# Kernel optimization log

Measured on AMD Instinct MI355X. Metric: run time of the kernel, lower is better.

Reference implementation:

```python
import jax, jax.numpy as jnp
import numpy as np

B, T, HID, NH = 2, 2048, 1024, 16
HD = HID // NH  # head_dim = 64
ROPE_BASE = 1000000.0


def _precompute_freqs(dim, end, rope_base):
    inv = 1.0 / (rope_base ** (np.arange(0, dim, 2)[: dim // 2].astype(np.float32) / dim))
    t = np.arange(end, dtype=np.float32)
    freqs = np.outer(t, inv).astype(np.float32)  # (end, dim//2)
    cos = np.concatenate([np.cos(freqs), np.cos(freqs)], axis=-1)
    sin = np.concatenate([np.sin(freqs), np.sin(freqs)], axis=-1)
    return jnp.asarray(cos), jnp.asarray(sin)


def setup_inputs() -> dict:
    key = jax.random.key(0)
    ks = jax.random.split(key, 5)
    x = jax.random.normal(ks[0], (B, T, HID), dtype=jnp.float32)
    s = 1.0 / np.sqrt(HID)
    Wq = jax.random.normal(ks[1], (HID, HID), dtype=jnp.float32) * s
    Wk = jax.random.normal(ks[2], (HID, HID), dtype=jnp.float32) * s
    Wv = jax.random.normal(ks[3], (HID, HID), dtype=jnp.float32) * s
    Wo = jax.random.normal(ks[4], (HID, HID), dtype=jnp.float32) * s
    cos, sin = _precompute_freqs(HD, T, ROPE_BASE)
    return {"x": x, "Wq": Wq, "Wk": Wk, "Wv": Wv, "Wo": Wo, "cos": cos, "sin": sin}


def _rotate_half(u):
    half = u.shape[-1] // 2
    return jnp.concatenate([-u[..., half:], u[..., :half]], axis=-1)


def reference(x, Wq, Wk, Wv, Wo, cos, sin):
    b, t, _ = x.shape
    # projections (nn.Linear: x @ W.T)
    q = (x @ Wq.T).reshape(b, t, NH, HD).transpose(0, 2, 1, 3)  # (B,H,T,D)
    k = (x @ Wk.T).reshape(b, t, NH, HD).transpose(0, 2, 1, 3)
    v = (x @ Wv.T).reshape(b, t, NH, HD).transpose(0, 2, 1, 3)
    c = cos[None, None, :t, :]
    s = sin[None, None, :t, :]
    q = q * c + _rotate_half(q) * s
    k = k * c + _rotate_half(k) * s
    scores = jnp.einsum("bhqd,bhkd->bhqk", q, k) / jnp.sqrt(jnp.float32(HD))
    causal = jnp.tril(jnp.ones((t, t), dtype=bool))
    scores = jnp.where(causal[None, None], scores, jnp.float32(-jnp.inf))
    prob = jax.nn.softmax(scores, axis=-1)
    out = jnp.einsum("bhqk,bhkd->bhqd", prob, v)
    out = out.transpose(0, 2, 1, 3).reshape(b, t, HID)
    return out @ Wo.T
```

## Files before the change

kernel.cpp:

```cpp
#include <hip/hip_runtime.h>
#include <hip/hip_bf16.h>

#define B_   2
#define T_   2048
#define HID_ 1024
#define NH_  16
#define HD_  64
#define K_   1024
#define M_   (B_*T_)

typedef __attribute__((ext_vector_type(8)))  short bf16x8;
typedef __attribute__((ext_vector_type(4)))  float f32x4;
typedef __attribute__((ext_vector_type(16))) float f32x16;
typedef __attribute__((ext_vector_type(4)))  unsigned int u32x4;
typedef __attribute__((ext_vector_type(2)))  unsigned int u32x2;

#define LOG2E 1.44269504088896340736f

__device__ inline unsigned short f2bf(float f) {
    __hip_bfloat16 h = __float2bfloat16(f);
    return __builtin_bit_cast(unsigned short, h);
}
__device__ inline unsigned int pk2(float a, float b) {
    return (unsigned int)f2bf(a) | ((unsigned int)f2bf(b) << 16);
}
__device__ inline unsigned int pkt(float a, float b) {
    return __builtin_amdgcn_perm(__builtin_bit_cast(unsigned, a),
                                 __builtin_bit_cast(unsigned, b), 0x03020706u);
}
__device__ inline bf16x8 cvt8(float4 a, float4 b) {
    bf16x8 r;
    r[0]=(short)f2bf(a.x); r[1]=(short)f2bf(a.y); r[2]=(short)f2bf(a.z); r[3]=(short)f2bf(a.w);
    r[4]=(short)f2bf(b.x); r[5]=(short)f2bf(b.y); r[6]=(short)f2bf(b.z); r[7]=(short)f2bf(b.w);
    return r;
}

__global__ __launch_bounds__(256)
void cast_all(const float* __restrict__ x,
              const float* __restrict__ W0, const float* __restrict__ W1,
              const float* __restrict__ W2, const float* __restrict__ W3,
              unsigned short* __restrict__ xo,
              unsigned short* __restrict__ o0, unsigned short* __restrict__ o1,
              unsigned short* __restrict__ o2, unsigned short* __restrict__ o3) {
    const int blk = blockIdx.x;
    const float* in;
    unsigned short* out;
    int i;
    if (blk < 2048) {
        in = x; out = xo; i = blk * 256 + threadIdx.x;
    } else {
        const int wb = blk - 2048, sec = wb >> 9;
        in  = (sec == 0) ? W0 : (sec == 1) ? W1 : (sec == 2) ? W2 : W3;
        out = (sec == 0) ? o0 : (sec == 1) ? o1 : (sec == 2) ? o2 : o3;
        i = (wb & 511) * 256 + threadIdx.x;
    }
    float4 a = ((const float4*)in)[2*i], b = ((const float4*)in)[2*i + 1];
    ((bf16x8*)out)[i] = cvt8(a, b);
}

template<int TYPE>
__global__ __launch_bounds__(256)
void gemm_k(const unsigned short* __restrict__ A, const unsigned short* __restrict__ W0,
            const unsigned short* __restrict__ W1, const unsigned short* __restrict__ W2,
            const float* __restrict__ cs, const float* __restrict__ sn,
            unsigned short* __restrict__ qb, unsigned short* __restrict__ kb,
            unsigned short* __restrict__ vtb, float* __restrict__ fout) {
    __shared__ unsigned short As[128*64];
    __shared__ unsigned short Bs[128*64];
    const int tid = threadIdx.x;
    const int w = tid >> 6, lane = tid & 63;
    const int u = lane >> 4, c = lane & 15;
    const int bm = blockIdx.x * 128, bn = blockIdx.y * 128;
    const int wm = (w & 1) * 64, wn = (w >> 1) * 64;
    const int srow = tid >> 3, scol = (tid & 7) << 3;

    const unsigned short* Wsec;
    int wrowbase;
    if constexpr (TYPE == 0) {
        const int sec = bn >> 10;
        Wsec = (sec == 0) ? W0 : ((sec == 1) ? W1 : W2);
        wrowbase = bn & 1023;
    } else {
        Wsec = W0;
        wrowbase = bn;
    }
    const unsigned short* Wp = Wsec + (size_t)(wrowbase + srow) * K_ + scol;
    const unsigned short* Ap = A + (size_t)(bm + srow) * K_ + scol;

    f32x4 acc[4][4] = {};
    bf16x8 ra[4], rb[4];

    auto loadin = [&](int k0) {
        #pragma unroll
        for (int i = 0; i < 4; ++i) {
            ra[i] = *(const bf16x8*)(Ap + (size_t)i * 32 * K_ + k0);
            rb[i] = *(const bf16x8*)(Wp + (size_t)i * 32 * K_ + k0);
        }
    };
    loadin(0);

    for (int k0 = 0; k0 < K_; k0 += 64) {
        __syncthreads();
        #pragma unroll
        for (int i = 0; i < 4; ++i) {
            const int row = i * 32 + srow;
            const int sc = (scol * 2) ^ ((row & 7) << 4);
            *(bf16x8*)((char*)As + row * 128 + sc) = ra[i];
            *(bf16x8*)((char*)Bs + row * 128 + sc) = rb[i];
        }
        __syncthreads();
        if (k0 < K_ - 64) loadin(k0 + 64);
        #pragma unroll
        for (int kk = 0; kk < 2; ++kk) {
            bf16x8 af[4], bfr[4];
            #pragma unroll
            for (int mi = 0; mi < 4; ++mi) {
                const int row = wm + mi * 16 + c;
                const int sc = (kk * 64 + u * 16) ^ ((row & 7) << 4);
                af[mi] = *(const bf16x8*)((char*)As + row * 128 + sc);
            }
            #pragma unroll
            for (int ni = 0; ni < 4; ++ni) {
                const int row = wn + ni * 16 + c;
                const int sc = (kk * 64 + u * 16) ^ ((row & 7) << 4);
                bfr[ni] = *(const bf16x8*)((char*)Bs + row * 128 + sc);
            }
            #pragma unroll
            for (int mi = 0; mi < 4; ++mi)
                #pragma unroll
                for (int ni = 0; ni < 4; ++ni)
                    acc[mi][ni] = __builtin_amdgcn_mfma_f32_16x16x32_bf16(
                        af[mi], bfr[ni], acc[mi][ni], 0, 0, 0);
        }
    }

    if constexpr (TYPE == 1) {
        #pragma unroll
        for (int mi = 0; mi < 4; ++mi)
            #pragma unroll
            for (int ni = 0; ni < 4; ++ni)
                #pragma unroll
                for (int r = 0; r < 4; ++r)
                    fout[(size_t)(bm + wm + 16*mi + 4*u + r) * HID_ + (bn + wn + 16*ni + c)] =
                        acc[mi][ni][r];
    } else {
        const int sec = bn >> 10;
        const int h = ((bn + wn) & 1023) >> 6;
        if (sec == 2) {
            #pragma unroll
            for (int mi = 0; mi < 4; ++mi)
                #pragma unroll
                for (int r = 0; r < 4; ++r) {
                    const int mg = bm + wm + 16*mi + 4*u + r;
                    const int bb = mg >> 11, t = mg & 2047;
                    const int tk = (t & ~12) | ((t & 4) << 1) | ((t & 8) >> 1);
                    #pragma unroll
                    for (int ni = 0; ni < 4; ++ni)
                        vtb[((size_t)(bb*16 + h) * 64 + 16*ni + c) * 2048 + tk] =
                            f2bf(acc[mi][ni][r]);
                }
        } else {
            unsigned short* ob = sec ? kb : qb;
            const float qsc = sec ? 1.0f : (0.125f * LOG2E);
            #pragma unroll
            for (int mi = 0; mi < 4; ++mi)
                #pragma unroll
                for (int r = 0; r < 4; ++r) {
                    const int mg = bm + wm + 16*mi + 4*u + r;
                    const int bb = mg >> 11, t = mg & 2047;
                    const size_t base = ((size_t)(bb*16 + h) * 2048 + t) * 64;
                    #pragma unroll
                    for (int ni = 0; ni < 2; ++ni) {
                        const int dlo = 16*ni + c;
                        const float cv = cs[t*64 + dlo], sv = sn[t*64 + dlo];
                        const float Aa = acc[mi][ni][r], Bb = acc[mi][ni+2][r];
                        ob[base + dlo]      = f2bf((Aa*cv - Bb*sv) * qsc);
                        ob[base + dlo + 32] = f2bf((Bb*cv + Aa*sv) * qsc);
                    }
                }
        }
    }
}

__global__ __launch_bounds__(256)
void attn11(const unsigned short* __restrict__ q, const unsigned short* __restrict__ k,
            const unsigned short* __restrict__ vt, unsigned short* __restrict__ ab) {
    const int raw = blockIdx.x;
    const int bh   = (raw & 7) + 8 * ((raw >> 3) & 3);
    const int qblk = 63 - (raw >> 5);
    const int tid = threadIdx.x;
    const int wid = tid >> 6, lane = tid & 63;
    const int h = lane >> 5, c = lane & 31;
    const int b = bh >> 4, hh = bh & 15;
    const int q0 = qblk * 32;
    const int qgc = q0 + c;
    const unsigned short* qp = q  + (size_t)bh * (T_*64);
    const unsigned short* kp = k  + (size_t)bh * (T_*64);
    const unsigned short* vp = vt + (size_t)bh * (64*T_);

    const int kloff  = c * 64 + 8 * h;
    const int vloff0 = c * 2048 + 8 * h;
    const int vloff1 = vloff0 + 32 * 2048;

    bf16x8 qf[4];
    {
        const unsigned short* qrow = qp + (q0 + c) * 64 + 8 * h;
        #pragma unroll
        for (int s = 0; s < 4; ++s)
            qf[s] = *(const bf16x8*)(qrow + s * 16);
    }

    f32x16 O0 = {}, O1 = {};
    float m = -1e30f, lsum = 0.f;
    const int nst = qblk + 1;

    auto loadKV = [&](bf16x8 (&kf)[4], bf16x8 (&vf)[4], int st) {
        const unsigned short* kst = kp + (st << 11);
        const unsigned short* vst = vp + (st << 5);
        #pragma unroll
        for (int s = 0; s < 4; ++s)
            kf[s] = *(const bf16x8*)(kst + kloff + s * 16);
        vf[0] = *(const bf16x8*)(vst + vloff0);
        vf[1] = *(const bf16x8*)(vst + vloff0 + 16);
        vf[2] = *(const bf16x8*)(vst + vloff1);
        vf[3] = *(const bf16x8*)(vst + vloff1 + 16);
    };

    auto process = [&](const bf16x8 (&kf)[4], const bf16x8 (&vf)[4], int st) {
        const int kvs = st << 5;
        __builtin_amdgcn_s_setprio(1);
        f32x16 sa = {};
        #pragma unroll
        for (int s = 0; s < 4; ++s)
            sa = __builtin_amdgcn_mfma_f32_32x32x16_bf16(kf[s], qf[s], sa, 0, 0, 0);
        __builtin_amdgcn_s_setprio(0);
        float p[16];
        #pragma unroll
        for (int r = 0; r < 16; ++r) p[r] = sa[r];
        if (st == qblk) {
            #pragma unroll
            for (int r = 0; r < 16; ++r) {
                const int kk = kvs + (r & 3) + 8 * (r >> 2) + 4 * h;
                if (kk > qgc) p[r] = -1e30f;
            }
        }
        const float a0 = fmaxf(fmaxf(p[0],  p[1]),  p[2]);
        const float a1 = fmaxf(fmaxf(p[3],  p[4]),  p[5]);
        const float a2 = fmaxf(fmaxf(p[6],  p[7]),  p[8]);
        const float a3 = fmaxf(fmaxf(p[9],  p[10]), p[11]);
        const float a4 = fmaxf(fmaxf(p[12], p[13]), p[14]);
        float mx = fmaxf(fmaxf(fmaxf(a0, a1), fmaxf(a2, a3)), fmaxf(a4, p[15]));
        if (!__all(mx <= m + 8.0f)) {
            mx = fmaxf(mx, __shfl_xor(mx, 32));
            const float mn = fmaxf(m, mx);
            const float f = __builtin_amdgcn_exp2f(m - mn);
            m = mn;
            lsum *= f;
            #pragma unroll
            for (int r = 0; r < 16; ++r) { O0[r] *= f; O1[r] *= f; }
        }
        float ps = 0.f;
        #pragma unroll
        for (int r = 0; r < 16; ++r) {
            p[r] = __builtin_amdgcn_exp2f(p[r] - m);
            ps += p[r];
        }
        lsum += ps;
        u32x4 B0w = { pkt(p[0],  p[1]),  pkt(p[2],  p[3]),
                      pkt(p[4],  p[5]),  pkt(p[6],  p[7])  };
        u32x4 B1w = { pkt(p[8],  p[9]),  pkt(p[10], p[11]),
                      pkt(p[12], p[13]), pkt(p[14], p[15]) };
        bf16x8 PB0 = __builtin_bit_cast(bf16x8, B0w);
        bf16x8 PB1 = __builtin_bit_cast(bf16x8, B1w);
        __builtin_amdgcn_s_setprio(1);
        O0 = __builtin_amdgcn_mfma_f32_32x32x16_bf16(vf[0], PB0, O0, 0, 0, 0);
        O0 = __builtin_amdgcn_mfma_f32_32x32x16_bf16(vf[1], PB1, O0, 0, 0, 0);
        O1 = __builtin_amdgcn_mfma_f32_32x32x16_bf16(vf[2], PB0, O1, 0, 0, 0);
        O1 = __builtin_amdgcn_mfma_f32_32x32x16_bf16(vf[3], PB1, O1, 0, 0, 0);
        __builtin_amdgcn_s_setprio(0);
    };

    bf16x8 kA[4], kB[4], vA[4], vB[4];
    if (wid < nst) loadKV(kA, vA, wid);
    for (int st = wid; st < nst; st += 8) {
        if (st + 4 < nst) loadKV(kB, vB, st + 4);
        process(kA, vA, st);
        if (st + 4 >= nst) break;
        if (st + 8 < nst) loadKV(kA, vA, st + 8);
        process(kB, vB, st + 4);
    }
    lsum += __shfl_xor(lsum, 32);

    __shared__ unsigned OSu[4][32 * 34];
    __shared__ float mS[4][32], lS[4][32];
    if (h == 0) { mS[wid][c] = m; lS[wid][c] = lsum; }
    {
        unsigned* os = &OSu[wid][0];
        const int rb = c * 34 + 2 * h;
        #pragma unroll
        for (int j = 0; j < 4; ++j) {
            os[rb + 4*j]          = pk2(O0[4*j],   O0[4*j+1]);
            os[rb + 4*j + 1]      = pk2(O0[4*j+2], O0[4*j+3]);
            os[rb + 16 + 4*j]     = pk2(O1[4*j],   O1[4*j+1]);
            os[rb + 16 + 4*j + 1] = pk2(O1[4*j+2], O1[4*j+3]);
        }
    }
    __syncthreads();

    const int ql = tid & 31, ug = (tid >> 5) * 4;
    const float M = fmaxf(fmaxf(mS[0][ql], mS[1][ql]), fmaxf(mS[2][ql], mS[3][ql]));
    float acc[8] = {};
    float L = 0.f;
    #pragma unroll
    for (int w2 = 0; w2 < 4; ++w2) {
        const float sc = __builtin_amdgcn_exp2f(mS[w2][ql] - M);
        L += lS[w2][ql] * sc;
        u32x2 pa = *(u32x2*)&OSu[w2][ql * 34 + ug];
        u32x2 pb = *(u32x2*)&OSu[w2][ql * 34 + ug + 2];
        #pragma unroll
        for (int t = 0; t < 2; ++t) {
            acc[2*t]     += __builtin_bit_cast(float, pa[t] << 16) * sc;
            acc[2*t+1]   += __builtin_bit_cast(float, pa[t] & 0xffff0000u) * sc;
            acc[4+2*t]   += __builtin_bit_cast(float, pb[t] << 16) * sc;
            acc[4+2*t+1] += __builtin_bit_cast(float, pb[t] & 0xffff0000u) * sc;
        }
    }
    const float inv = 1.0f / L;
    uint4 ov;
    ov.x = pk2(acc[0]*inv, acc[1]*inv);
    ov.y = pk2(acc[2]*inv, acc[3]*inv);
    ov.z = pk2(acc[4]*inv, acc[5]*inv);
    ov.w = pk2(acc[6]*inv, acc[7]*inv);
    *(uint4*)(ab + ((size_t)(b * T_) + q0 + ql) * HID_ + hh * 64 + ug * 2) = ov;
}

extern "C" void kernel_launch(void* const* d_in, const int* in_sizes, int n_in,
                              void* d_out, int out_size, void* d_ws, size_t ws_size,
                              hipStream_t stream) {
    const float* x  = (const float*)d_in[0];
    const float* Wq = (const float*)d_in[1];
    const float* Wk = (const float*)d_in[2];
    const float* Wv = (const float*)d_in[3];
    const float* Wo = (const float*)d_in[4];
    const float* cs = (const float*)d_in[5];
    const float* sn = (const float*)d_in[6];
    char* wsb = (char*)d_ws;
    unsigned short* xb  = (unsigned short*)(wsb);
    unsigned short* wqb = (unsigned short*)(wsb + (8u  << 20));
    unsigned short* wkb = (unsigned short*)(wsb + (10u << 20));
    unsigned short* wvb = (unsigned short*)(wsb + (12u << 20));
    unsigned short* wob = (unsigned short*)(wsb + (14u << 20));
    unsigned short* qb  = (unsigned short*)(wsb + (16u << 20));
    unsigned short* kb  = (unsigned short*)(wsb + (24u << 20));
    unsigned short* vtb = (unsigned short*)(wsb + (32u << 20));
    unsigned short* ab  = (unsigned short*)(wsb + (40u << 20));

    cast_all<<<4096, 256, 0, stream>>>(x, Wq, Wk, Wv, Wo, xb, wqb, wkb, wvb, wob);

    gemm_k<0><<<dim3(M_/128, 3072/128), 256, 0, stream>>>(
        xb, wqb, wkb, wvb, cs, sn, qb, kb, vtb, nullptr);
    attn11<<<2048, 256, 0, stream>>>(qb, kb, vtb, ab);
    gemm_k<1><<<dim3(M_/128, HID_/128), 256, 0, stream>>>(
        ab, wob, nullptr, nullptr, nullptr, nullptr,
        nullptr, nullptr, nullptr, (float*)d_out);
}
```

Measured before the change: 127.8 us.

## Process three query tiles per attention block, remap GEMM blocks across XCDs

The attention kernel now has each block handle 96 query rows as three 32-row tiles that share one K/V load per key step. This cuts K/V global traffic and block count (704 blocks instead of 2048), at the cost of more registers and uneven causal work per tile. Both GEMMs move to a 1D grid with an XCD-aware swizzle of block indices, meant to improve L2 locality. The output projection GEMM also switches to 128x64 tiles so it launches more blocks.

```diff
diff --git a/kernel.cpp b/kernel.cpp
--- a/kernel.cpp
+++ b/kernel.cpp
@@ -65,13 +65,26 @@
             const float* __restrict__ cs, const float* __restrict__ sn,
             unsigned short* __restrict__ qb, unsigned short* __restrict__ kb,
             unsigned short* __restrict__ vtb, float* __restrict__ fout) {
+    constexpr int BN = (TYPE == 1) ? 64 : 128;
+    constexpr int NB = BN / 32;
+    constexpr int NF = BN / 32;
     __shared__ unsigned short As[128*64];
-    __shared__ unsigned short Bs[128*64];
+    __shared__ unsigned short Bs[BN*64];
     const int tid = threadIdx.x;
     const int w = tid >> 6, lane = tid & 63;
     const int u = lane >> 4, c = lane & 15;
-    const int bm = blockIdx.x * 128, bn = blockIdx.y * 128;
-    const int wm = (w & 1) * 64, wn = (w >> 1) * 64;
+    const int bid = blockIdx.x;
+    const int xcd = bid & 7, idx = bid >> 3;
+    int bmi, bni;
+    if constexpr (TYPE == 0) {
+        bmi = (xcd & 3) * 8 + (idx & 7);
+        bni = (xcd >> 2) * 12 + (idx >> 3);
+    } else {
+        bmi = (xcd & 3) * 8 + (idx & 7);
+        bni = (xcd >> 2) * 8 + (idx >> 3);
+    }
+    const int bm = bmi * 128, bn = bni * BN;
+    const int wm = (w & 1) * 64, wn = (w >> 1) * (BN / 2);
     const int srow = tid >> 3, scol = (tid & 7) << 3;
 
     const unsigned short* Wsec;
@@ -87,15 +100,16 @@
     const unsigned short* Wp = Wsec + (size_t)(wrowbase + srow) * K_ + scol;
     const unsigned short* Ap = A + (size_t)(bm + srow) * K_ + scol;
 
-    f32x4 acc[4][4] = {};
-    bf16x8 ra[4], rb[4];
+    f32x4 acc[4][NF] = {};
+    bf16x8 ra[4], rb[NB];
 
     auto loadin = [&](int k0) {
         #pragma unroll
-        for (int i = 0; i < 4; ++i) {
+        for (int i = 0; i < 4; ++i)
             ra[i] = *(const bf16x8*)(Ap + (size_t)i * 32 * K_ + k0);
+        #pragma unroll
+        for (int i = 0; i < NB; ++i)
             rb[i] = *(const bf16x8*)(Wp + (size_t)i * 32 * K_ + k0);
-        }
     };
     loadin(0);
 
@@ -106,13 +120,18 @@
             const int row = i * 32 + srow;
             const int sc = (scol * 2) ^ ((row & 7) << 4);
             *(bf16x8*)((char*)As + row * 128 + sc) = ra[i];
+        }
+        #pragma unroll
+        for (int i = 0; i < NB; ++i) {
+            const int row = i * 32 + srow;
+            const int sc = (scol * 2) ^ ((row & 7) << 4);
             *(bf16x8*)((char*)Bs + row * 128 + sc) = rb[i];
         }
         __syncthreads();
         if (k0 < K_ - 64) loadin(k0 + 64);
         #pragma unroll
         for (int kk = 0; kk < 2; ++kk) {
-            bf16x8 af[4], bfr[4];
+            bf16x8 af[4], bfr[NF];
             #pragma unroll
             for (int mi = 0; mi < 4; ++mi) {
                 const int row = wm + mi * 16 + c;
@@ -120,7 +139,7 @@
                 af[mi] = *(const bf16x8*)((char*)As + row * 128 + sc);
             }
             #pragma unroll
-            for (int ni = 0; ni < 4; ++ni) {
+            for (int ni = 0; ni < NF; ++ni) {
                 const int row = wn + ni * 16 + c;
                 const int sc = (kk * 64 + u * 16) ^ ((row & 7) << 4);
                 bfr[ni] = *(const bf16x8*)((char*)Bs + row * 128 + sc);
@@ -128,7 +147,7 @@
             #pragma unroll
             for (int mi = 0; mi < 4; ++mi)
                 #pragma unroll
-                for (int ni = 0; ni < 4; ++ni)
+                for (int ni = 0; ni < NF; ++ni)
                     acc[mi][ni] = __builtin_amdgcn_mfma_f32_16x16x32_bf16(
                         af[mi], bfr[ni], acc[mi][ni], 0, 0, 0);
         }
@@ -138,7 +157,7 @@
         #pragma unroll
         for (int mi = 0; mi < 4; ++mi)
             #pragma unroll
-            for (int ni = 0; ni < 4; ++ni)
+            for (int ni = 0; ni < NF; ++ni)
                 #pragma unroll
                 for (int r = 0; r < 4; ++r)
                     fout[(size_t)(bm + wm + 16*mi + 4*u + r) * HID_ + (bn + wn + 16*ni + c)] =
@@ -183,17 +202,21 @@
 }
 
 __global__ __launch_bounds__(256)
-void attn11(const unsigned short* __restrict__ q, const unsigned short* __restrict__ k,
+void attn17(const unsigned short* __restrict__ q, const unsigned short* __restrict__ k,
             const unsigned short* __restrict__ vt, unsigned short* __restrict__ ab) {
     const int raw = blockIdx.x;
-    const int bh   = (raw & 7) + 8 * ((raw >> 3) & 3);
-    const int qblk = 63 - (raw >> 5);
+    const int bh     = (raw & 7) + 8 * ((raw >> 3) & 3);
+    const int qchunk = 21 - (raw >> 5);
+    const bool hasBC = (qchunk < 21);
     const int tid = threadIdx.x;
     const int wid = tid >> 6, lane = tid & 63;
     const int h = lane >> 5, c = lane & 31;
     const int b = bh >> 4, hh = bh & 15;
-    const int q0 = qblk * 32;
-    const int qgc = q0 + c;
+    const int q0 = qchunk * 96;
+    const int qgcA = q0 + c, qgcB = q0 + 32 + c, qgcC = q0 + 64 + c;
+    const int stAd = 3 * qchunk;
+    const int stBd = stAd + 1, stCd = stAd + 2;
+    const int NT   = hasBC ? (stAd + 3) : (stAd + 1);
     const unsigned short* qp = q  + (size_t)bh * (T_*64);
     const unsigned short* kp = k  + (size_t)bh * (T_*64);
     const unsigned short* vp = vt + (size_t)bh * (64*T_);
@@ -202,42 +225,39 @@
     const int vloff0 = c * 2048 + 8 * h;
     const int vloff1 = vloff0 + 32 * 2048;
 
-    bf16x8 qf[4];
+    bf16x8 qfA[4], qfB[4], qfC[4];
     {
-        const unsigned short* qrow = qp + (q0 + c) * 64 + 8 * h;
-        #pragma unroll
-        for (int s = 0; s < 4; ++s)
-            qf[s] = *(const bf16x8*)(qrow + s * 16);
-    }
-
-    f32x16 O0 = {}, O1 = {};
-    float m = -1e30f, lsum = 0.f;
-    const int nst = qblk + 1;
-
-    auto loadKV = [&](bf16x8 (&kf)[4], bf16x8 (&vf)[4], int st) {
+        const unsigned short* qrowA = qp + (q0 + c) * 64 + 8 * h;
+        #pragma unroll
+        for (int s = 0; s < 4; ++s) qfA[s] = *(const bf16x8*)(qrowA + s * 16);
+        if (hasBC) {
+            #pragma unroll
+            for (int s = 0; s < 4; ++s) {
+                qfB[s] = *(const bf16x8*)(qrowA + 32 * 64 + s * 16);
+                qfC[s] = *(const bf16x8*)(qrowA + 64 * 64 + s * 16);
+            }
+        }
+    }
+
+    f32x16 OA0 = {}, OA1 = {}, OB0 = {}, OB1 = {}, OC0 = {}, OC1 = {};
+    float mA = -1e30f, lA = 0.f, mB = -1e30f, lB = 0.f, mC = -1e30f, lC = 0.f;
+
+    auto loadK = [&](bf16x8 (&kf)[4], int st) {
         const unsigned short* kst = kp + (st << 11);
-        const unsigned short* vst = vp + (st << 5);
         #pragma unroll
         for (int s = 0; s < 4; ++s)
             kf[s] = *(const bf16x8*)(kst + kloff + s * 16);
-        vf[0] = *(const bf16x8*)(vst + vloff0);
-        vf[1] = *(const bf16x8*)(vst + vloff0 + 16);
-        vf[2] = *(const bf16x8*)(vst + vloff1);
-        vf[3] = *(const bf16x8*)(vst + vloff1 + 16);
     };
 
-    auto process = [&](const bf16x8 (&kf)[4], const bf16x8 (&vf)[4], int st) {
+    auto tileRest = [&](f32x16 sa, int st, int std_, int qgc,
+                        float& m, float& l, f32x16& O0, f32x16& O1,
+                        const bf16x8& vf0, const bf16x8& vf1,
+                        const bf16x8& vf2, const bf16x8& vf3) {
         const int kvs = st << 5;
-        __builtin_amdgcn_s_setprio(1);
-        f32x16 sa = {};
-        #pragma unroll
-        for (int s = 0; s < 4; ++s)
-            sa = __builtin_amdgcn_mfma_f32_32x32x16_bf16(kf[s], qf[s], sa, 0, 0, 0);
-        __builtin_amdgcn_s_setprio(0);
         float p[16];
         #pragma unroll
         for (int r = 0; r < 16; ++r) p[r] = sa[r];
-        if (st == qblk) {
+        if (st == std_) {
             #pragma unroll
             for (int r = 0; r < 16; ++r) {
                 const int kk = kvs + (r & 3) + 8 * (r >> 2) + 4 * h;
@@ -254,8 +274,7 @@
             mx = fmaxf(mx, __shfl_xor(mx, 32));
             const float mn = fmaxf(m, mx);
             const float f = __builtin_amdgcn_exp2f(m - mn);
-            m = mn;
-            lsum *= f;
+            m = mn; l *= f;
             #pragma unroll
             for (int r = 0; r < 16; ++r) { O0[r] *= f; O1[r] *= f; }
         }
@@ -265,7 +284,7 @@
             p[r] = __builtin_amdgcn_exp2f(p[r] - m);
             ps += p[r];
         }
-        lsum += ps;
+        l += ps;
         u32x4 B0w = { pkt(p[0],  p[1]),  pkt(p[2],  p[3]),
                       pkt(p[4],  p[5]),  pkt(p[6],  p[7])  };
         u32x4 B1w = { pkt(p[8],  p[9]),  pkt(p[10], p[11]),
@@ -273,65 +292,111 @@
         bf16x8 PB0 = __builtin_bit_cast(bf16x8, B0w);
         bf16x8 PB1 = __builtin_bit_cast(bf16x8, B1w);
         __builtin_amdgcn_s_setprio(1);
-        O0 = __builtin_amdgcn_mfma_f32_32x32x16_bf16(vf[0], PB0, O0, 0, 0, 0);
-        O0 = __builtin_amdgcn_mfma_f32_32x32x16_bf16(vf[1], PB1, O0, 0, 0, 0);
-        O1 = __builtin_amdgcn_mfma_f32_32x32x16_bf16(vf[2], PB0, O1, 0, 0, 0);
-        O1 = __builtin_amdgcn_mfma_f32_32x32x16_bf16(vf[3], PB1, O1, 0, 0, 0);
+        O0 = __builtin_amdgcn_mfma_f32_32x32x16_bf16(vf0, PB0, O0, 0, 0, 0);
+        O0 = __builtin_amdgcn_mfma_f32_32x32x16_bf16(vf1, PB1, O0, 0, 0, 0);
+        O1 = __builtin_amdgcn_mfma_f32_32x32x16_bf16(vf2, PB0, O1, 0, 0, 0);
+        O1 = __builtin_amdgcn_mfma_f32_32x32x16_bf16(vf3, PB1, O1, 0, 0, 0);
         __builtin_amdgcn_s_setprio(0);
     };
 
-    bf16x8 kA[4], kB[4], vA[4], vB[4];
-    if (wid < nst) loadKV(kA, vA, wid);
-    for (int st = wid; st < nst; st += 8) {
-        if (st + 4 < nst) loadKV(kB, vB, st + 4);
-        process(kA, vA, st);
-        if (st + 4 >= nst) break;
-        if (st + 8 < nst) loadKV(kA, vA, st + 8);
-        process(kB, vB, st + 4);
-    }
-    lsum += __shfl_xor(lsum, 32);
-
-    __shared__ unsigned OSu[4][32 * 34];
-    __shared__ float mS[4][32], lS[4][32];
-    if (h == 0) { mS[wid][c] = m; lS[wid][c] = lsum; }
+    auto qkt = [&](const bf16x8 (&kf)[4], const bf16x8 (&qf)[4]) -> f32x16 {
+        __builtin_amdgcn_s_setprio(1);
+        f32x16 sa = {};
+        #pragma unroll
+        for (int s = 0; s < 4; ++s)
+            sa = __builtin_amdgcn_mfma_f32_32x32x16_bf16(kf[s], qf[s], sa, 0, 0, 0);
+        __builtin_amdgcn_s_setprio(0);
+        return sa;
+    };
+
+    bf16x8 kf_[4];
+    if (wid < NT) {
+        loadK(kf_, wid);
+        for (int st = wid; st < NT; st += 4) {
+            const unsigned short* vst = vp + (st << 5);
+            bf16x8 vf0 = *(const bf16x8*)(vst + vloff0);
+            bf16x8 vf1 = *(const bf16x8*)(vst + vloff0 + 16);
+            bf16x8 vf2 = *(const bf16x8*)(vst + vloff1);
+            bf16x8 vf3 = *(const bf16x8*)(vst + vloff1 + 16);
+            const bool doA = (st <= stAd);
+            const bool doB = hasBC && (st <= stBd);
+            if (doA) {
+                f32x16 sa = qkt(kf_, qfA);
+                if (!hasBC && st + 4 < NT) loadK(kf_, st + 4);
+                tileRest(sa, st, stAd, qgcA, mA, lA, OA0, OA1, vf0, vf1, vf2, vf3);
+            }
+            if (doB) {
+                f32x16 sa = qkt(kf_, qfB);
+                tileRest(sa, st, stBd, qgcB, mB, lB, OB0, OB1, vf0, vf1, vf2, vf3);
+            }
+            if (hasBC) {
+                f32x16 sa = qkt(kf_, qfC);
+                if (st + 4 < NT) loadK(kf_, st + 4);
+                tileRest(sa, st, stCd, qgcC, mC, lC, OC0, OC1, vf0, vf1, vf2, vf3);
+            }
+        }
+    }
+    lA += __shfl_xor(lA, 32);
+    lB += __shfl_xor(lB, 32);
+    lC += __shfl_xor(lC, 32);
+
+    __shared__ unsigned OSu[4][96 * 34];
+    __shared__ float mS[4][96], lS[4][96];
+    if (h == 0) {
+        mS[wid][c] = mA;      lS[wid][c] = lA;
+        mS[wid][32 + c] = mB; lS[wid][32 + c] = lB;
+        mS[wid][64 + c] = mC; lS[wid][64 + c] = lC;
+    }
     {
         unsigned* os = &OSu[wid][0];
-        const int rb = c * 34 + 2 * h;
+        const int rbA = c * 34 + 2 * h;
+        const int rbB = (32 + c) * 34 + 2 * h;
+        const int rbC = (64 + c) * 34 + 2 * h;
         #pragma unroll
         for (int j = 0; j < 4; ++j) {
-            os[rb + 4*j]          = pk2(O0[4*j],   O0[4*j+1]);
-            os[rb + 4*j + 1]      = pk2(O0[4*j+2], O0[4*j+3]);
-            os[rb + 16 + 4*j]     = pk2(O1[4*j],   O1[4*j+1]);
-            os[rb + 16 + 4*j + 1] = pk2(O1[4*j+2], O1[4*j+3]);
+            os[rbA + 4*j]          = pk2(OA0[4*j],   OA0[4*j+1]);
+            os[rbA + 4*j + 1]      = pk2(OA0[4*j+2], OA0[4*j+3]);
+            os[rbA + 16 + 4*j]     = pk2(OA1[4*j],   OA1[4*j+1]);
+            os[rbA + 16 + 4*j + 1] = pk2(OA1[4*j+2], OA1[4*j+3]);
+            os[rbB + 4*j]          = pk2(OB0[4*j],   OB0[4*j+1]);
+            os[rbB + 4*j + 1]      = pk2(OB0[4*j+2], OB0[4*j+3]);
+            os[rbB + 16 + 4*j]     = pk2(OB1[4*j],   OB1[4*j+1]);
+            os[rbB + 16 + 4*j + 1] = pk2(OB1[4*j+2], OB1[4*j+3]);
+            os[rbC + 4*j]          = pk2(OC0[4*j],   OC0[4*j+1]);
+            os[rbC + 4*j + 1]      = pk2(OC0[4*j+2], OC0[4*j+3]);
+            os[rbC + 16 + 4*j]     = pk2(OC1[4*j],   OC1[4*j+1]);
+            os[rbC + 16 + 4*j + 1] = pk2(OC1[4*j+2], OC1[4*j+3]);
         }
     }
     __syncthreads();
 
-    const int ql = tid & 31, ug = (tid >> 5) * 4;
-    const float M = fmaxf(fmaxf(mS[0][ql], mS[1][ql]), fmaxf(mS[2][ql], mS[3][ql]));
-    float acc[8] = {};
-    float L = 0.f;
     #pragma unroll
-    for (int w2 = 0; w2 < 4; ++w2) {
-        const float sc = __builtin_amdgcn_exp2f(mS[w2][ql] - M);
-        L += lS[w2][ql] * sc;
-        u32x2 pa = *(u32x2*)&OSu[w2][ql * 34 + ug];
-        u32x2 pb = *(u32x2*)&OSu[w2][ql * 34 + ug + 2];
-        #pragma unroll
-        for (int t = 0; t < 2; ++t) {
-            acc[2*t]     += __builtin_bit_cast(float, pa[t] << 16) * sc;
-            acc[2*t+1]   += __builtin_bit_cast(float, pa[t] & 0xffff0000u) * sc;
-            acc[4+2*t]   += __builtin_bit_cast(float, pb[t] << 16) * sc;
-            acc[4+2*t+1] += __builtin_bit_cast(float, pb[t] & 0xffff0000u) * sc;
-        }
-    }
-    const float inv = 1.0f / L;
-    uint4 ov;
-    ov.x = pk2(acc[0]*inv, acc[1]*inv);
-    ov.y = pk2(acc[2]*inv, acc[3]*inv);
-    ov.z = pk2(acc[4]*inv, acc[5]*inv);
-    ov.w = pk2(acc[6]*inv, acc[7]*inv);
-    *(uint4*)(ab + ((size_t)(b * T_) + q0 + ql) * HID_ + hh * 64 + ug * 2) = ov;
+    for (int rr = 0; rr < 3; ++rr) {
+        if (rr > 0 && !hasBC) break;
+        const int rl = rr * 32 + (tid & 31);
+        const int ug = (tid >> 5) * 4;
+        const float M = fmaxf(fmaxf(mS[0][rl], mS[1][rl]), fmaxf(mS[2][rl], mS[3][rl]));
+        float acc[8] = {};
+        float L = 0.f;
+        #pragma unroll
+        for (int w2 = 0; w2 < 4; ++w2) {
+            const float sc = __builtin_amdgcn_exp2f(mS[w2][rl] - M);
+            L += lS[w2][rl] * sc;
+            u32x4 pa = *(u32x4*)&OSu[w2][rl * 34 + ug];
+            #pragma unroll
+            for (int t = 0; t < 4; ++t) {
+                acc[2*t]   += __builtin_bit_cast(float, pa[t] << 16) * sc;
+                acc[2*t+1] += __builtin_bit_cast(float, pa[t] & 0xffff0000u) * sc;
+            }
+        }
+        const float inv = 1.0f / L;
+        uint4 ov;
+        ov.x = pk2(acc[0]*inv, acc[1]*inv);
+        ov.y = pk2(acc[2]*inv, acc[3]*inv);
+        ov.z = pk2(acc[4]*inv, acc[5]*inv);
+        ov.w = pk2(acc[6]*inv, acc[7]*inv);
+        *(uint4*)(ab + ((size_t)(b * T_) + q0 + rl) * HID_ + hh * 64 + ug * 2) = ov;
+    }
 }
 
 extern "C" void kernel_launch(void* const* d_in, const int* in_sizes, int n_in,
@@ -357,10 +422,10 @@
 
     cast_all<<<4096, 256, 0, stream>>>(x, Wq, Wk, Wv, Wo, xb, wqb, wkb, wvb, wob);
 
-    gemm_k<0><<<dim3(M_/128, 3072/128), 256, 0, stream>>>(
+    gemm_k<0><<<768, 256, 0, stream>>>(
         xb, wqb, wkb, wvb, cs, sn, qb, kb, vtb, nullptr);
-    attn11<<<2048, 256, 0, stream>>>(qb, kb, vtb, ab);
-    gemm_k<1><<<dim3(M_/128, HID_/128), 256, 0, stream>>>(
+    attn17<<<704, 256, 0, stream>>>(qb, kb, vtb, ab);
+    gemm_k<1><<<512, 256, 0, stream>>>(
         ab, wob, nullptr, nullptr, nullptr, nullptr,
         nullptr, nullptr, nullptr, (float*)d_out);
 }
```

Measured after the change: 113.9 us. 1.12x faster.
